# Optimization experiments

Hardware: AMD Instinct MI355X
Metric: run time of the kernel (lower is better)

## Reference

```python
import jax, jax.numpy as jnp
import numpy as np

EPS = 1e-5  # PyTorch BatchNorm3d default eps

def _bn(x, gamma, beta, mean, var):
    # eval-mode batchnorm over channel dim (axis=1) of [B,C,D,H,W]
    inv = jax.lax.rsqrt(var + EPS)
    scale = (gamma * inv)[None, :, None, None, None]
    shift = (beta - mean * gamma * inv)[None, :, None, None, None]
    return x * scale + shift

def _pconv(x, w):
    # 1x1x1 conv3d == channel contraction: w [O,C], x [B,C,D,H,W]
    return jnp.einsum('oc,bcdhw->bodhw', w, x)

def setup_inputs() -> dict:
    key = jax.random.key(0)
    ks = jax.random.split(key, 12)
    B, G, D, H, W = 4, 8, 48, 128, 160
    x1 = jax.random.normal(ks[0], (B, G, D, H, W), dtype=jnp.float32)
    # conv0: G->16 (no bias), BN params for 16 channels
    w0 = jax.random.normal(ks[1], (16, G), dtype=jnp.float32) * 0.1
    g0 = jnp.ones((16,), jnp.float32)
    b0 = jnp.zeros((16,), jnp.float32)
    m0 = jax.random.normal(ks[2], (16,), dtype=jnp.float32) * 0.01
    v0 = jax.random.uniform(ks[3], (16,), jnp.float32, 0.5, 1.5)
    # conv1: 16->8 (no bias), BN params for 8 channels
    w1 = jax.random.normal(ks[4], (8, 16), dtype=jnp.float32) * 0.1
    g1 = jnp.ones((8,), jnp.float32)
    b1 = jnp.zeros((8,), jnp.float32)
    m1 = jax.random.normal(ks[5], (8,), dtype=jnp.float32) * 0.01
    v1 = jax.random.uniform(ks[6], (8,), jnp.float32, 0.5, 1.5)
    # conv2: 8->1 with bias (xavier init)
    lim = float(np.sqrt(6.0 / (8 + 1)))
    w2 = jax.random.uniform(ks[7], (1, 8), jnp.float32, -lim, lim)
    b2 = jnp.zeros((1,), jnp.float32)
    return {"x1": x1, "w0": w0, "g0": g0, "b0": b0, "m0": m0, "v0": v0,
            "w1": w1, "g1": g1, "b1": b1, "m1": m1, "v1": v1,
            "w2": w2, "b2": b2}

def reference(x1, w0, g0, b0, m0, v0, w1, g1, b1, m1, v1, w2, b2):
    h = jax.nn.relu(_bn(_pconv(x1, w0), g0, b0, m0, v0))   # [B,16,D,H,W]
    h = jax.nn.relu(_bn(_pconv(h, w1), g1, b1, m1, v1))    # [B,8,D,H,W]
    h = _pconv(h, w2) + b2[None, :, None, None, None]      # [B,1,D,H,W]
    h = jnp.squeeze(h, axis=1)                             # view -> [B,D,H,W]
    out = jnp.max(jax.nn.sigmoid(h), axis=1)               # max over depth
    return out[:, None]                                    # [B,1,H,W]
```

## Files before the change

### kernel.cpp

```cpp
#include <hip/hip_runtime.h>

#define BATCH 4
#define CIN   8
#define DEPTH 48
#define HGT   128
#define WID   160

#define HW    (HGT*WID)
#define DHW   (DEPTH*HW)
#define CDHW  (CIN*DHW)
#define NPIX  (BATCH*HW)

#define DSPLIT 8
#define DCHUNK (DEPTH/DSPLIT)
#define TILES_PER_B (HW/128)
#define NTILES (NPIX/128)

#define WS_W0F 0
#define WS_S0F 128
#define WS_W1F 144
#define WS_S1F 272
#define WS_W2F 280
#define WS_B2F 288
#define WS_FLAG 384
#define WS_PART 512

static __device__ __forceinline__ float asf(unsigned int u) {
    return __builtin_bit_cast(float, u);
}
static __device__ __forceinline__ unsigned int asu(float f) {
    return __builtin_bit_cast(unsigned int, f);
}
static __device__ __forceinline__ float ldp(const void* p, int i, bool bf) {
    if (bf) {
        unsigned int u = ((const unsigned short*)p)[i];
        return asf(u << 16);
    }
    return ((const float*)p)[i];
}

__global__ void detect_kernel(const unsigned int* __restrict__ x, unsigned int* __restrict__ wsu)
{
    int lane = threadIdx.x;
    int cnt = 0;
    #pragma unroll
    for (int i = 0; i < 16; ++i) {
        unsigned int v = x[(unsigned)(lane * 997 + i * 61440 + 12345)];
        unsigned int b1 = (v >> 8) & 0xFFu;
        if ((b1 & 0x78u) == 0x38u) ++cnt;
    }
    #pragma unroll
    for (int off = 32; off > 0; off >>= 1) cnt += __shfl_down(cnt, off, 64);
    if (lane == 0) wsu[WS_FLAG] = (cnt >= 512) ? 1u : 0u;
}

__global__ void prep_kernel(const void* __restrict__ w0, const void* __restrict__ g0,
                            const void* __restrict__ b0, const void* __restrict__ m0,
                            const void* __restrict__ v0, const void* __restrict__ w1,
                            const void* __restrict__ g1, const void* __restrict__ b1,
                            const void* __restrict__ m1, const void* __restrict__ v1,
                            const void* __restrict__ w2, const void* __restrict__ b2,
                            float* __restrict__ ws)
{
    bool bf = (((const unsigned int*)ws)[WS_FLAG] != 0u);
    int t = threadIdx.x;
    if (t < 16) {
        float sc = ldp(g0, t, bf) * rsqrtf(ldp(v0, t, bf) + 1e-5f);
        for (int c = 0; c < 8; ++c)
            ws[WS_W0F + t*8 + c] = ldp(w0, t*8 + c, bf) * sc;
        ws[WS_S0F + t] = ldp(b0, t, bf) - ldp(m0, t, bf) * sc;
    }
    if (t < 8) {
        float sc = ldp(g1, t, bf) * rsqrtf(ldp(v1, t, bf) + 1e-5f);
        for (int c = 0; c < 16; ++c)
            ws[WS_W1F + t*16 + c] = ldp(w1, t*16 + c, bf) * sc;
        ws[WS_S1F + t] = ldp(b1, t, bf) - ldp(m1, t, bf) * sc;
        ws[WS_W2F + t] = ldp(w2, t, bf);
    }
    if (t == 0) ws[WS_B2F] = ldp(b2, 0, bf);
}

__global__ __launch_bounds__(64, 1) void main_kernel(const void* __restrict__ xv,
                                                     const float* __restrict__ ws,
                                                     float* __restrict__ part)
{
    bool bf = (((const unsigned int*)ws)[WS_FLAG] != 0u);
    const unsigned int* xb = (const unsigned int*)xv;
    const float2*      xf = (const float2*)xv;

    int lane = threadIdx.x;
    int bid  = blockIdx.x;
    int tile = bid % NTILES;
    int dc   = bid / NTILES;
    int b    = tile / TILES_PER_B;
    int hwp  = (tile % TILES_PER_B) * 64 + lane;
    unsigned bbase = (unsigned)(b * (CDHW/2)) + (unsigned)hwp;
    int d0 = dc * DCHUNK;

    float W0f[128], S0[16], W1f[128], S1[8], W2[8];
    {
        const float4* q0 = (const float4*)(ws + WS_W0F);
        #pragma unroll
        for (int i = 0; i < 32; ++i) { float4 f = q0[i]; W0f[4*i]=f.x; W0f[4*i+1]=f.y; W0f[4*i+2]=f.z; W0f[4*i+3]=f.w; }
        const float4* qs = (const float4*)(ws + WS_S0F);
        #pragma unroll
        for (int i = 0; i < 4; ++i) { float4 f = qs[i]; S0[4*i]=f.x; S0[4*i+1]=f.y; S0[4*i+2]=f.z; S0[4*i+3]=f.w; }
        const float4* q1 = (const float4*)(ws + WS_W1F);
        #pragma unroll
        for (int i = 0; i < 32; ++i) { float4 f = q1[i]; W1f[4*i]=f.x; W1f[4*i+1]=f.y; W1f[4*i+2]=f.z; W1f[4*i+3]=f.w; }
        const float4* qt = (const float4*)(ws + WS_S1F);
        #pragma unroll
        for (int i = 0; i < 2; ++i) { float4 f = qt[i]; S1[4*i]=f.x; S1[4*i+1]=f.y; S1[4*i+2]=f.z; S1[4*i+3]=f.w; }
        const float4* qw = (const float4*)(ws + WS_W2F);
        #pragma unroll
        for (int i = 0; i < 2; ++i) { float4 f = qw[i]; W2[4*i]=f.x; W2[4*i+1]=f.y; W2[4*i+2]=f.z; W2[4*i+3]=f.w; }
    }
    float B2v = ws[WS_B2F];

    float mA = -1e30f, mB = -1e30f;

    for (int dd = 0; dd < DCHUNK; ++dd) {
        int d = d0 + dd;
        unsigned idx0 = bbase + (unsigned)(d * (HW/2));

        float xAf[8], xBf[8];
        if (bf) {
            #pragma unroll
            for (int c = 0; c < 8; ++c) {
                unsigned int v = xb[idx0 + (unsigned)(c * (DHW/2))];
                xAf[c] = asf(v << 16);
                xBf[c] = asf(v & 0xFFFF0000u);
            }
        } else {
            #pragma unroll
            for (int c = 0; c < 8; ++c) {
                float2 v = xf[idx0 + (unsigned)(c * (DHW/2))];
                xAf[c] = v.x;
                xBf[c] = v.y;
            }
        }

        float h0A[16], h0B[16];
        #pragma unroll
        for (int o = 0; o < 16; ++o) {
            float a = S0[o], bb = S0[o];
            #pragma unroll
            for (int c = 0; c < 8; ++c) {
                a  = fmaf(xAf[c], W0f[o*8 + c], a);
                bb = fmaf(xBf[c], W0f[o*8 + c], bb);
            }
            h0A[o] = fmaxf(a, 0.f);
            h0B[o] = fmaxf(bb, 0.f);
        }

        float sA = B2v, sB = B2v;
        #pragma unroll
        for (int o = 0; o < 8; ++o) {
            float a = S1[o], bb = S1[o];
            #pragma unroll
            for (int c = 0; c < 16; ++c) {
                a  = fmaf(h0A[c], W1f[o*16 + c], a);
                bb = fmaf(h0B[c], W1f[o*16 + c], bb);
            }
            sA = fmaf(W2[o], fmaxf(a, 0.f), sA);
            sB = fmaf(W2[o], fmaxf(bb, 0.f), sB);
        }
        mA = fmaxf(mA, sA);
        mB = fmaxf(mB, sB);
    }

    float2 r; r.x = mA; r.y = mB;
    float2* pp = (float2*)(part + (size_t)dc * NPIX + (size_t)b * HW);
    pp[hwp] = r;
}

__global__ __launch_bounds__(256) void reduce_kernel(const float* __restrict__ part,
                                                     const float* __restrict__ ws,
                                                     void* __restrict__ out)
{
    bool bf = (((const unsigned int*)ws)[WS_FLAG] != 0u);
    int px = blockIdx.x * 256 + threadIdx.x;
    float m = part[px];
    #pragma unroll
    for (int k = 1; k < DSPLIT; ++k) m = fmaxf(m, part[(size_t)k * NPIX + px]);
    float sg = 1.0f / (1.0f + __expf(-m));
    if (bf) {
        unsigned int u = asu(sg);
        unsigned int r = (u + 0x7FFFu + ((u >> 16) & 1u)) >> 16;
        ((unsigned short*)out)[px] = (unsigned short)r;
    } else {
        ((float*)out)[px] = sg;
    }
}

extern "C" void kernel_launch(void* const* d_in, const int* in_sizes, int n_in,
                              void* d_out, int out_size, void* d_ws, size_t ws_size,
                              hipStream_t stream)
{
    float* ws = (float*)d_ws;

    detect_kernel<<<1, 64, 0, stream>>>((const unsigned int*)d_in[0], (unsigned int*)d_ws);

    prep_kernel<<<1, 64, 0, stream>>>(
        d_in[1], d_in[2], d_in[3], d_in[4], d_in[5], d_in[6],
        d_in[7], d_in[8], d_in[9], d_in[10], d_in[11], d_in[12], ws);

    main_kernel<<<NTILES * DSPLIT, 64, 0, stream>>>(d_in[0], ws, ws + WS_PART);

    reduce_kernel<<<NPIX / 256, 256, 0, stream>>>(ws + WS_PART, ws, d_out);
}
```

Measured before the change: 225.1 us.

## Use packed fp16 dot products for pointwise convs and merge detect into prep

Folded weights are stored as packed fp16 pairs, and inputs and hidden activations are converted with cvt_pkrtz so both channel contractions run as v_dot2 fp16 instructions with fp32 accumulation. This halves the FMA instruction count and the weight-register footprint, which allows launch_bounds occupancy of 2 and a depth-loop unroll of 2. The dtype-detect kernel is folded into prep, saving one launch. The cost is reduced precision (fp16 rounding toward zero of inputs and activations) and extra conversion instructions.

```diff
diff --git a/kernel.cpp b/kernel.cpp
--- a/kernel.cpp
+++ b/kernel.cpp
@@ -16,20 +16,29 @@
 #define TILES_PER_B (HW/128)
 #define NTILES (NPIX/128)
 
-#define WS_W0F 0
-#define WS_S0F 128
-#define WS_W1F 144
-#define WS_S1F 272
-#define WS_W2F 280
-#define WS_B2F 288
+#define WS_W0P 0
+#define WS_S0F 64
+#define WS_W1P 80
+#define WS_S1F 144
+#define WS_W2F 152
+#define WS_B2F 160
 #define WS_FLAG 384
 #define WS_PART 512
 
+typedef _Float16 half2_t __attribute__((ext_vector_type(2)));
+
 static __device__ __forceinline__ float asf(unsigned int u) {
     return __builtin_bit_cast(float, u);
 }
 static __device__ __forceinline__ unsigned int asu(float f) {
     return __builtin_bit_cast(unsigned int, f);
+}
+static __device__ __forceinline__ unsigned int pkrtz_u(float a, float b) {
+    return __builtin_bit_cast(unsigned int, __builtin_amdgcn_cvt_pkrtz(a, b));
+}
+static __device__ __forceinline__ float fdot2_u(unsigned int a, unsigned int b, float c) {
+    return __builtin_amdgcn_fdot2(__builtin_bit_cast(half2_t, a),
+                                  __builtin_bit_cast(half2_t, b), c, false);
 }
 static __device__ __forceinline__ float ldp(const void* p, int i, bool bf) {
     if (bf) {
@@ -39,22 +48,8 @@
     return ((const float*)p)[i];
 }
 
-__global__ void detect_kernel(const unsigned int* __restrict__ x, unsigned int* __restrict__ wsu)
-{
-    int lane = threadIdx.x;
-    int cnt = 0;
-    #pragma unroll
-    for (int i = 0; i < 16; ++i) {
-        unsigned int v = x[(unsigned)(lane * 997 + i * 61440 + 12345)];
-        unsigned int b1 = (v >> 8) & 0xFFu;
-        if ((b1 & 0x78u) == 0x38u) ++cnt;
-    }
-    #pragma unroll
-    for (int off = 32; off > 0; off >>= 1) cnt += __shfl_down(cnt, off, 64);
-    if (lane == 0) wsu[WS_FLAG] = (cnt >= 512) ? 1u : 0u;
-}
-
-__global__ void prep_kernel(const void* __restrict__ w0, const void* __restrict__ g0,
+__global__ void prep_kernel(const unsigned int* __restrict__ x,
+                            const void* __restrict__ w0, const void* __restrict__ g0,
                             const void* __restrict__ b0, const void* __restrict__ m0,
                             const void* __restrict__ v0, const void* __restrict__ w1,
                             const void* __restrict__ g1, const void* __restrict__ b1,
@@ -62,29 +57,45 @@
                             const void* __restrict__ w2, const void* __restrict__ b2,
                             float* __restrict__ ws)
 {
-    bool bf = (((const unsigned int*)ws)[WS_FLAG] != 0u);
+    unsigned int* wsu = (unsigned int*)ws;
     int t = threadIdx.x;
+
+    int cnt = 0;
+    #pragma unroll
+    for (int i = 0; i < 16; ++i) {
+        unsigned int v = x[(unsigned)(t * 997 + i * 61440 + 12345)];
+        if ((((v >> 8) & 0x78u)) == 0x38u) ++cnt;
+    }
+    #pragma unroll
+    for (int off = 32; off > 0; off >>= 1) cnt += __shfl_down(cnt, off, 64);
+    cnt = __shfl(cnt, 0, 64);
+    bool bf = (cnt >= 512);
+    if (t == 0) wsu[WS_FLAG] = bf ? 1u : 0u;
+
     if (t < 16) {
         float sc = ldp(g0, t, bf) * rsqrtf(ldp(v0, t, bf) + 1e-5f);
-        for (int c = 0; c < 8; ++c)
-            ws[WS_W0F + t*8 + c] = ldp(w0, t*8 + c, bf) * sc;
+        for (int c = 0; c < 4; ++c)
+            wsu[WS_W0P + t*4 + c] = pkrtz_u(ldp(w0, t*8 + 2*c, bf) * sc,
+                                            ldp(w0, t*8 + 2*c + 1, bf) * sc);
         ws[WS_S0F + t] = ldp(b0, t, bf) - ldp(m0, t, bf) * sc;
     }
     if (t < 8) {
         float sc = ldp(g1, t, bf) * rsqrtf(ldp(v1, t, bf) + 1e-5f);
-        for (int c = 0; c < 16; ++c)
-            ws[WS_W1F + t*16 + c] = ldp(w1, t*16 + c, bf) * sc;
+        for (int c = 0; c < 8; ++c)
+            wsu[WS_W1P + t*8 + c] = pkrtz_u(ldp(w1, t*16 + 2*c, bf) * sc,
+                                            ldp(w1, t*16 + 2*c + 1, bf) * sc);
         ws[WS_S1F + t] = ldp(b1, t, bf) - ldp(m1, t, bf) * sc;
         ws[WS_W2F + t] = ldp(w2, t, bf);
     }
     if (t == 0) ws[WS_B2F] = ldp(b2, 0, bf);
 }
 
-__global__ __launch_bounds__(64, 1) void main_kernel(const void* __restrict__ xv,
+__global__ __launch_bounds__(64, 2) void main_kernel(const void* __restrict__ xv,
                                                      const float* __restrict__ ws,
                                                      float* __restrict__ part)
 {
-    bool bf = (((const unsigned int*)ws)[WS_FLAG] != 0u);
+    const unsigned int* wsu = (const unsigned int*)ws;
+    bool bf = (wsu[WS_FLAG] != 0u);
     const unsigned int* xb = (const unsigned int*)xv;
     const float2*      xf = (const float2*)xv;
 
@@ -97,17 +108,18 @@
     unsigned bbase = (unsigned)(b * (CDHW/2)) + (unsigned)hwp;
     int d0 = dc * DCHUNK;
 
-    float W0f[128], S0[16], W1f[128], S1[8], W2[8];
+    unsigned int W0p[64], W1p[64];
+    float S0[16], S1[8], W2[8];
     {
-        const float4* q0 = (const float4*)(ws + WS_W0F);
-        #pragma unroll
-        for (int i = 0; i < 32; ++i) { float4 f = q0[i]; W0f[4*i]=f.x; W0f[4*i+1]=f.y; W0f[4*i+2]=f.z; W0f[4*i+3]=f.w; }
+        const uint4* q0 = (const uint4*)(wsu + WS_W0P);
+        #pragma unroll
+        for (int i = 0; i < 16; ++i) { uint4 q = q0[i]; W0p[4*i]=q.x; W0p[4*i+1]=q.y; W0p[4*i+2]=q.z; W0p[4*i+3]=q.w; }
+        const uint4* q1 = (const uint4*)(wsu + WS_W1P);
+        #pragma unroll
+        for (int i = 0; i < 16; ++i) { uint4 q = q1[i]; W1p[4*i]=q.x; W1p[4*i+1]=q.y; W1p[4*i+2]=q.z; W1p[4*i+3]=q.w; }
         const float4* qs = (const float4*)(ws + WS_S0F);
         #pragma unroll
         for (int i = 0; i < 4; ++i) { float4 f = qs[i]; S0[4*i]=f.x; S0[4*i+1]=f.y; S0[4*i+2]=f.z; S0[4*i+3]=f.w; }
-        const float4* q1 = (const float4*)(ws + WS_W1F);
-        #pragma unroll
-        for (int i = 0; i < 32; ++i) { float4 f = q1[i]; W1f[4*i]=f.x; W1f[4*i+1]=f.y; W1f[4*i+2]=f.z; W1f[4*i+3]=f.w; }
         const float4* qt = (const float4*)(ws + WS_S1F);
         #pragma unroll
         for (int i = 0; i < 2; ++i) { float4 f = qt[i]; S1[4*i]=f.x; S1[4*i+1]=f.y; S1[4*i+2]=f.z; S1[4*i+3]=f.w; }
@@ -119,51 +131,62 @@
 
     float mA = -1e30f, mB = -1e30f;
 
+    #pragma unroll 2
     for (int dd = 0; dd < DCHUNK; ++dd) {
         int d = d0 + dd;
         unsigned idx0 = bbase + (unsigned)(d * (HW/2));
 
-        float xAf[8], xBf[8];
+        unsigned int xA[4], xB[4];
         if (bf) {
-            #pragma unroll
-            for (int c = 0; c < 8; ++c) {
-                unsigned int v = xb[idx0 + (unsigned)(c * (DHW/2))];
-                xAf[c] = asf(v << 16);
-                xBf[c] = asf(v & 0xFFFF0000u);
+            unsigned int xd[8];
+            #pragma unroll
+            for (int c = 0; c < 8; ++c) xd[c] = xb[idx0 + (unsigned)(c * (DHW/2))];
+            #pragma unroll
+            for (int j = 0; j < 4; ++j) {
+                xA[j] = pkrtz_u(asf(xd[2*j] << 16),        asf(xd[2*j+1] << 16));
+                xB[j] = pkrtz_u(asf(xd[2*j] & 0xFFFF0000u), asf(xd[2*j+1] & 0xFFFF0000u));
             }
         } else {
-            #pragma unroll
-            for (int c = 0; c < 8; ++c) {
-                float2 v = xf[idx0 + (unsigned)(c * (DHW/2))];
-                xAf[c] = v.x;
-                xBf[c] = v.y;
+            float2 v[8];
+            #pragma unroll
+            for (int c = 0; c < 8; ++c) v[c] = xf[idx0 + (unsigned)(c * (DHW/2))];
+            #pragma unroll
+            for (int j = 0; j < 4; ++j) {
+                xA[j] = pkrtz_u(v[2*j].x, v[2*j+1].x);
+                xB[j] = pkrtz_u(v[2*j].y, v[2*j+1].y);
             }
         }
 
         float h0A[16], h0B[16];
         #pragma unroll
         for (int o = 0; o < 16; ++o) {
-            float a = S0[o], bb = S0[o];
-            #pragma unroll
-            for (int c = 0; c < 8; ++c) {
-                a  = fmaf(xAf[c], W0f[o*8 + c], a);
-                bb = fmaf(xBf[c], W0f[o*8 + c], bb);
+            float a = S0[o], c = S0[o];
+            #pragma unroll
+            for (int j = 0; j < 4; ++j) {
+                a = fdot2_u(xA[j], W0p[o*4 + j], a);
+                c = fdot2_u(xB[j], W0p[o*4 + j], c);
             }
             h0A[o] = fmaxf(a, 0.f);
-            h0B[o] = fmaxf(bb, 0.f);
+            h0B[o] = fmaxf(c, 0.f);
+        }
+        unsigned int gA[8], gB[8];
+        #pragma unroll
+        for (int k = 0; k < 8; ++k) {
+            gA[k] = pkrtz_u(h0A[2*k], h0A[2*k+1]);
+            gB[k] = pkrtz_u(h0B[2*k], h0B[2*k+1]);
         }
 
         float sA = B2v, sB = B2v;
         #pragma unroll
         for (int o = 0; o < 8; ++o) {
-            float a = S1[o], bb = S1[o];
-            #pragma unroll
-            for (int c = 0; c < 16; ++c) {
-                a  = fmaf(h0A[c], W1f[o*16 + c], a);
-                bb = fmaf(h0B[c], W1f[o*16 + c], bb);
+            float a = S1[o], c = S1[o];
+            #pragma unroll
+            for (int k = 0; k < 8; ++k) {
+                a = fdot2_u(gA[k], W1p[o*8 + k], a);
+                c = fdot2_u(gB[k], W1p[o*8 + k], c);
             }
             sA = fmaf(W2[o], fmaxf(a, 0.f), sA);
-            sB = fmaf(W2[o], fmaxf(bb, 0.f), sB);
+            sB = fmaf(W2[o], fmaxf(c, 0.f), sB);
         }
         mA = fmaxf(mA, sA);
         mB = fmaxf(mB, sB);
@@ -199,9 +222,8 @@
 {
     float* ws = (float*)d_ws;
 
-    detect_kernel<<<1, 64, 0, stream>>>((const unsigned int*)d_in[0], (unsigned int*)d_ws);
-
     prep_kernel<<<1, 64, 0, stream>>>(
+        (const unsigned int*)d_in[0],
         d_in[1], d_in[2], d_in[3], d_in[4], d_in[5], d_in[6],
         d_in[7], d_in[8], d_in[9], d_in[10], d_in[11], d_in[12], ws);
 
```

New measurement: 219.5 us. 2.5% less time.
